# Performance work log

Measured on AMD Instinct MI355X. Metric: run time of the kernel, lower is better.

The kernel has to match this reference:

```python
import jax, jax.numpy as jnp
import numpy as np

PATCH = 16      # sqrt(n_patches=256)
ALPHA = 10.0
HEADS, DH = 2, 64


def _fourier(coords, Bm):
    # coords: (HW, 2), Bm: (n_features, 2) -> (HW, 2*n_features)
    proj = 2.0 * jnp.pi * coords @ Bm.T
    return jnp.concatenate([jnp.cos(proj), jnp.sin(proj)], axis=-1)


def _forward(coords_decoding, tokens, B_q, B_l0, B_l1,
             qW, qb, toqW, tokvW, tooW, toob,
             bwW0, bwb0, bwW1, bwb1,
             modW0, modb0, modW1, modb1,
             hvW0, hvb0, outW0, outb0, outW1, outb1):
    B = coords_decoding.shape[0]
    Hh, Ww = coords_decoding.shape[1], coords_decoding.shape[2]
    coords = coords_decoding.reshape(B, -1, coords_decoding.shape[-1])
    grid = coords[0]                      # (HW, 2); coords_modulation is None -> same grid
    HW = grid.shape[0]
    m = tokens.shape[1]

    # patch indices and spatial bias
    row = jnp.clip((grid[:, 0] * PATCH).astype(jnp.int32), 0, PATCH - 1)
    col = jnp.clip((grid[:, 1] * PATCH).astype(jnp.int32), 0, PATCH - 1)
    idx = row * PATCH + col               # (HW,)
    t = idx.astype(jnp.float32) / (PATCH * PATCH)
    pos = (jnp.arange(m, dtype=jnp.float32) + 0.5) / m
    rel = -ALPHA * jnp.abs(t[None, :] - pos[:, None]) ** 2   # (m, HW)
    bias = rel.T                          # (HW, m), broadcast over batch & heads

    # query features (shared across batch)
    xq = jax.nn.relu(_fourier(grid, B_q) @ qW + qb)           # (HW, hd)
    xq_b = jnp.broadcast_to(xq[None], (B, HW, xq.shape[-1]))

    # cross attention with spatial bias
    q = (xq_b @ toqW).reshape(B, HW, HEADS, DH).transpose(0, 2, 1, 3)   # (B,h,HW,Dh)
    kv = tokens @ tokvW                                                  # (B,m,2*inner)
    k, v = jnp.split(kv, 2, axis=-1)
    k = k.reshape(B, m, HEADS, DH).transpose(0, 2, 1, 3)                 # (B,h,m,Dh)
    v = v.reshape(B, m, HEADS, DH).transpose(0, 2, 1, 3)
    sim = jnp.einsum('bhqd,bhkd->bhqk', q, k) * (DH ** -0.5) + bias[None, None]
    attn = jax.nn.softmax(sim, axis=-1)
    o = jnp.einsum('bhqk,bhkd->bhqd', attn, v)
    o = o.transpose(0, 2, 1, 3).reshape(B, HW, HEADS * DH)
    mod = o @ tooW + toob                                                # (B,HW,hd)

    # per-band MLP stack (layer_num = 2)
    def band(Bl, bwW, bwb, mW, mb):
        h = jax.nn.relu(_fourier(grid, Bl) @ bwW + bwb)                  # (HW,hd)
        return jax.nn.relu(h[None] + mod @ mW + mb)                      # (B,HW,hd)

    m0 = band(B_l0, bwW0, bwb0, modW0, modb0)
    m1 = band(B_l1, bwW1, bwb1, modW1, modb1)
    hv0 = m0
    hv1 = jax.nn.relu((m1 + hv0) @ hvW0 + hvb0)
    out = (hv0 @ outW0 + outb0) + (hv1 @ outW1 + outb1)                  # (B,HW,3)
    return out.reshape(B, Hh, Ww, -1)


def setup_inputs() -> dict:
    key = jax.random.key(0)
    ks = jax.random.split(key, 32)
    B, H, W, L = 4, 128, 128, 256
    fd, hd, cd, od = 64, 256, 256, 3
    nf = fd // 2
    inner = HEADS * DH

    def lin(k, i, o):
        return jax.random.normal(k, (i, o), dtype=jnp.float32) / np.sqrt(i).astype(np.float32)

    inp = {}
    inp['coords_decoding'] = jax.random.uniform(ks[0], (B, H, W, 2), dtype=jnp.float32)
    inp['tokens'] = jax.random.normal(ks[1], (B, L, cd), dtype=jnp.float32)
    inp['B_q'] = jax.random.normal(ks[2], (nf, 2), dtype=jnp.float32) / 16.0
    inp['B_l0'] = jax.random.normal(ks[3], (nf, 2), dtype=jnp.float32) / 128.0
    inp['B_l1'] = jax.random.normal(ks[4], (nf, 2), dtype=jnp.float32) / 32.0
    inp['qW'] = lin(ks[5], fd, hd); inp['qb'] = jnp.zeros((hd,), jnp.float32)
    inp['toqW'] = lin(ks[6], hd, inner)
    inp['tokvW'] = lin(ks[7], cd, inner * 2)
    inp['tooW'] = lin(ks[8], inner, hd); inp['toob'] = jnp.zeros((hd,), jnp.float32)
    inp['bwW0'] = lin(ks[9], fd, hd); inp['bwb0'] = jnp.zeros((hd,), jnp.float32)
    inp['bwW1'] = lin(ks[10], fd, hd); inp['bwb1'] = jnp.zeros((hd,), jnp.float32)
    inp['modW0'] = lin(ks[11], hd, hd); inp['modb0'] = jnp.zeros((hd,), jnp.float32)
    inp['modW1'] = lin(ks[12], hd, hd); inp['modb1'] = jnp.zeros((hd,), jnp.float32)
    inp['hvW0'] = lin(ks[13], hd, hd); inp['hvb0'] = jnp.zeros((hd,), jnp.float32)
    inp['outW0'] = lin(ks[14], hd, od); inp['outb0'] = jnp.zeros((od,), jnp.float32)
    inp['outW1'] = lin(ks[15], hd, od); inp['outb1'] = jnp.zeros((od,), jnp.float32)
    return inp


def reference(coords_decoding, tokens, B_q, B_l0, B_l1,
              qW, qb, toqW, tokvW, tooW, toob,
              bwW0, bwb0, bwW1, bwb1,
              modW0, modb0, modW1, modb1,
              hvW0, hvb0, outW0, outb0, outW1, outb1):
    return _forward(coords_decoding, tokens, B_q, B_l0, B_l1,
                    qW, qb, toqW, tokvW, tooW, toob,
                    bwW0, bwb0, bwW1, bwb1,
                    modW0, modb0, modW1, modb1,
                    hvW0, hvb0, outW0, outb0, outW1, outb1)
```

## Files before the change

kernel.cpp:

```cpp
#include <hip/hip_runtime.h>
#include <stdint.h>

constexpr int kHW = 16384;
constexpr int kB  = 4;
constexpr int kM  = 256;

typedef _Float16 half8 __attribute__((ext_vector_type(8)));
typedef __attribute__((ext_vector_type(4))) float f32x4;

__device__ __forceinline__ unsigned short f2h(float f) {
  _Float16 h = (_Float16)f;
  return __builtin_bit_cast(unsigned short, h);
}
__device__ __forceinline__ float h2f(unsigned short u) {
  return (float)__builtin_bit_cast(_Float16, u);
}

__global__ __launch_bounds__(256) void prep_kernel(
    const float* __restrict__ tokens, const float* __restrict__ tokvW,
    unsigned short* __restrict__ kn_ws, unsigned short* __restrict__ vt_ws,
    const float* __restrict__ tooW, const float* __restrict__ modW0,
    const float* __restrict__ modW1, const float* __restrict__ hvW0,
    const float* __restrict__ qW, const float* __restrict__ bwW0,
    const float* __restrict__ bwW1, const float* __restrict__ toqW,
    unsigned short* __restrict__ tooWt, unsigned short* __restrict__ modW0t,
    unsigned short* __restrict__ modW1t, unsigned short* __restrict__ hvW0t,
    unsigned short* __restrict__ qWt, unsigned short* __restrict__ bw0t,
    unsigned short* __restrict__ bw1t, unsigned short* __restrict__ toqWt)
{
  __shared__ __align__(16) float tok[256];
  int bx = blockIdx.x, tid = threadIdx.x;

  if (bx < kB * kM) {
    int b = bx >> 8, j = bx & 255, c = tid;
    tok[c] = tokens[(b * kM + j) * 256 + c];
    __syncthreads();
    float acc = 0.f;
    for (int i4 = 0; i4 < 64; i4++) {
      float4 t4 = *(const float4*)&tok[i4 * 4];
      acc += t4.x * tokvW[(i4*4+0)*256 + c] + t4.y * tokvW[(i4*4+1)*256 + c]
           + t4.z * tokvW[(i4*4+2)*256 + c] + t4.w * tokvW[(i4*4+3)*256 + c];
    }
    unsigned short hv = f2h(acc);
    if (c < 128) {
      int h = c >> 6, dd = c & 63;
      kn_ws[((size_t)(b*2+h)*256 + j) * 64 + dd] = hv;
    } else {
      int c2 = c - 128;
      int h = c2 >> 6, dd = c2 & 63;
      vt_ws[((size_t)(b*2+h)*64 + dd) * 256 + j] = hv;
    }
  } else {
    int t = bx - kB * kM;
    int m = t >> 3, ch = t & 7;
    const float* Ws[8] = {tooW, modW0, modW1, hvW0, qW, bwW0, bwW1, toqW};
    unsigned short* Wts[8] = {tooWt, modW0t, modW1t, hvW0t, qWt, bw0t, bw1t, toqWt};
    const int Ks[8] = {128, 256, 256, 256, 64, 64, 64, 256};
    const int Ns[8] = {256, 256, 256, 256, 256, 256, 256, 128};
    const float* W = Ws[m];
    unsigned short* Wt = Wts[m];
    int K = Ks[m], N = Ns[m];
    int nkb = K / 8;
    int per = nkb >> 3;
    int kb0 = ch * per;
    if (tid < N) {
      for (int kb = kb0; kb < kb0 + per; kb++) {
        unsigned short sv[8];
#pragma unroll
        for (int i = 0; i < 8; i++)
          sv[i] = f2h(W[(kb * 8 + i) * N + tid]);
        *(uint4*)&Wt[tid * K + kb * 8] = *(const uint4*)sv;
      }
    }
  }
}

constexpr int kFPitch = 72;
constexpr int kXPitch = 264;

__global__ __launch_bounds__(256, 2) void feat_kernel(
    const float* __restrict__ coords,
    const float* __restrict__ Bq, const float* __restrict__ Bl0, const float* __restrict__ Bl1,
    const float* __restrict__ qb, const float* __restrict__ bwb0, const float* __restrict__ bwb1,
    const unsigned short* __restrict__ qWt, const unsigned short* __restrict__ bw0t,
    const unsigned short* __restrict__ bw1t, const unsigned short* __restrict__ toqWt,
    float* __restrict__ t_ws, unsigned short* __restrict__ qc_ws,
    unsigned short* __restrict__ h0_hf, unsigned short* __restrict__ h1_hf)
{
  __shared__ __align__(16) unsigned short ff_s[3][32][kFPitch];
  __shared__ __align__(16) unsigned short xq_s[32][kXPitch];
  __shared__ float coords_s[64];

  int tid = threadIdx.x;
  int px0 = blockIdx.x * 32;
  int w = tid >> 6, ln = tid & 63;
  int c = ln & 15, q = ln >> 4;

  if (tid < 64) coords_s[tid] = coords[px0 * 2 + tid];
  __syncthreads();

#pragma unroll
  for (int r = 0; r < 24; r++) {
    int v = r * 256 + tid;
    int mat = v >> 11;
    int p = (v >> 6) & 31;
    int f = v & 63;
    int fr = f & 31;
    const float* Bm = (mat == 0) ? Bq : (mat == 1 ? Bl0 : Bl1);
    float x = coords_s[p * 2 + 0];
    float y = coords_s[p * 2 + 1];
    float proj = 6.283185307179586f * (x * Bm[fr*2+0] + y * Bm[fr*2+1]);
    float s, cc;
    __sincosf(proj, &s, &cc);
    ff_s[mat][p][f] = f2h((f < 32) ? cc : s);
  }
  if (tid < 32) {
    float x = coords_s[tid * 2 + 0];
    float y = coords_s[tid * 2 + 1];
    int row = min(max((int)(x * 16.0f), 0), 15);
    int col = min(max((int)(y * 16.0f), 0), 15);
    t_ws[px0 + tid] = (float)(row * 16 + col) * (1.0f / 256.0f);
  }
  __syncthreads();

  const f32x4 zero4 = {0.f, 0.f, 0.f, 0.f};

  for (int mat = 0; mat < 3; mat++) {
    const unsigned short* Wt = (mat == 0) ? qWt : (mat == 1 ? bw0t : bw1t);
    const float* bias = (mat == 0) ? qb : (mat == 1 ? bwb0 : bwb1);
    f32x4 acc[8];
#pragma unroll
    for (int i = 0; i < 8; i++) acc[i] = zero4;
#pragma unroll
    for (int ks = 0; ks < 2; ks++) {
      int koff = ks * 32 + q * 8;
      half8 bfr[4];
#pragma unroll
      for (int nt = 0; nt < 4; nt++)
        bfr[nt] = *(const half8*)(Wt + (size_t)(w*64 + nt*16 + c) * 64 + koff);
      half8 afr[2];
#pragma unroll
      for (int mt = 0; mt < 2; mt++)
        afr[mt] = *(const half8*)(&ff_s[mat][mt*16 + c][koff]);
#pragma unroll
      for (int mt = 0; mt < 2; mt++)
#pragma unroll
        for (int nt = 0; nt < 4; nt++)
          acc[mt*4+nt] = __builtin_amdgcn_mfma_f32_16x16x32_f16(afr[mt], bfr[nt], acc[mt*4+nt], 0, 0, 0);
    }
    float bv[4];
#pragma unroll
    for (int nt = 0; nt < 4; nt++) bv[nt] = bias[w*64 + nt*16 + c];
#pragma unroll
    for (int mt = 0; mt < 2; mt++)
#pragma unroll
      for (int nt = 0; nt < 4; nt++)
#pragma unroll
        for (int rg = 0; rg < 4; rg++) {
          int row = mt*16 + q*4 + rg, col = w*64 + nt*16 + c;
          unsigned short hv = f2h(fmaxf(acc[mt*4+nt][rg] + bv[nt], 0.f));
          if (mat == 0)      xq_s[row][col] = hv;
          else if (mat == 1) h0_hf[((size_t)(px0 + row)) * 256 + col] = hv;
          else               h1_hf[((size_t)(px0 + row)) * 256 + col] = hv;
        }
  }
  __syncthreads();

  {
    f32x4 acc2[4];
#pragma unroll
    for (int i = 0; i < 4; i++) acc2[i] = zero4;
#pragma unroll
    for (int kt = 0; kt < 8; kt++) {
      int koff = kt * 32 + q * 8;
      half8 bfr[2];
#pragma unroll
      for (int nt = 0; nt < 2; nt++)
        bfr[nt] = *(const half8*)(toqWt + (size_t)(w*32 + nt*16 + c) * 256 + koff);
      half8 afr[2];
#pragma unroll
      for (int mt = 0; mt < 2; mt++)
        afr[mt] = *(const half8*)(&xq_s[mt*16 + c][koff]);
#pragma unroll
      for (int mt = 0; mt < 2; mt++)
#pragma unroll
        for (int nt = 0; nt < 2; nt++)
          acc2[mt*2+nt] = __builtin_amdgcn_mfma_f32_16x16x32_f16(afr[mt], bfr[nt], acc2[mt*2+nt], 0, 0, 0);
    }
#pragma unroll
    for (int mt = 0; mt < 2; mt++)
#pragma unroll
      for (int nt = 0; nt < 2; nt++)
#pragma unroll
        for (int rg = 0; rg < 4; rg++) {
          int row = mt*16 + q*4 + rg, col = w*32 + nt*16 + c;
          qc_ws[((size_t)(px0 + row)) * 128 + col] = f2h(acc2[mt*2+nt][rg]);
        }
  }
}

constexpr int kPPitch = 264;

__global__ __launch_bounds__(256, 2) void attn_kernel(
    const unsigned short* __restrict__ kn_ws,
    const unsigned short* __restrict__ vt_ws,
    const unsigned short* __restrict__ qc_ws,
    const float* __restrict__ t_ws,
    unsigned short* __restrict__ o_hf)
{
  __shared__ __align__(16) unsigned short P_s[32 * kPPitch];
  __shared__ float t_s[32];
  __shared__ float red_max[32][4];
  __shared__ float red_sum[32][4];

  int b = blockIdx.y;
  int px0 = blockIdx.x * 32;
  int tid = threadIdx.x;
  int w = tid >> 6, ln = tid & 63;
  int c = ln & 15, q = ln >> 4;

  if (tid < 32) t_s[tid] = t_ws[px0 + tid];

  const f32x4 zero4 = {0.f, 0.f, 0.f, 0.f};

  for (int h = 0; h < 2; h++) {
    __syncthreads();

    f32x4 acc[8];
#pragma unroll
    for (int i = 0; i < 8; i++) acc[i] = zero4;
    const unsigned short* kbase = kn_ws + (size_t)(b*2+h) * 256 * 64;
#pragma unroll
    for (int ks = 0; ks < 2; ks++) {
      int koff = ks * 32 + q * 8;
      half8 a0 = *(const half8*)(qc_ws + (size_t)(px0 + c) * 128 + h*64 + koff);
      half8 a1 = *(const half8*)(qc_ws + (size_t)(px0 + 16 + c) * 128 + h*64 + koff);
#pragma unroll
      for (int nt = 0; nt < 4; nt++) {
        half8 bf = *(const half8*)(kbase + (size_t)(w*64 + nt*16 + c) * 64 + koff);
        acc[0*4+nt] = __builtin_amdgcn_mfma_f32_16x16x32_f16(a0, bf, acc[0*4+nt], 0, 0, 0);
        acc[1*4+nt] = __builtin_amdgcn_mfma_f32_16x16x32_f16(a1, bf, acc[1*4+nt], 0, 0, 0);
      }
    }

    float lm[2][4];
#pragma unroll
    for (int mt = 0; mt < 2; mt++)
#pragma unroll
      for (int rg = 0; rg < 4; rg++) {
        int row = mt*16 + q*4 + rg;
        float tv = t_s[row];
        float mx = -1e30f;
#pragma unroll
        for (int nt = 0; nt < 4; nt++) {
          int token = w*64 + nt*16 + c;
          float pos = ((float)token + 0.5f) * (1.0f / 256.0f);
          float db = tv - pos;
          float sb = acc[mt*4+nt][rg] * 0.125f - 10.0f * db * db;
          acc[mt*4+nt][rg] = sb;
          mx = fmaxf(mx, sb);
        }
        lm[mt][rg] = mx;
      }
#pragma unroll
    for (int s = 1; s < 16; s <<= 1)
#pragma unroll
      for (int mt = 0; mt < 2; mt++)
#pragma unroll
        for (int rg = 0; rg < 4; rg++)
          lm[mt][rg] = fmaxf(lm[mt][rg], __shfl_xor(lm[mt][rg], s, 64));
    if (c == 0) {
#pragma unroll
      for (int mt = 0; mt < 2; mt++)
#pragma unroll
        for (int rg = 0; rg < 4; rg++)
          red_max[mt*16 + q*4 + rg][w] = lm[mt][rg];
    }
    __syncthreads();

    float ps[2][4];
#pragma unroll
    for (int mt = 0; mt < 2; mt++)
#pragma unroll
      for (int rg = 0; rg < 4; rg++) {
        int row = mt*16 + q*4 + rg;
        float gm = fmaxf(fmaxf(red_max[row][0], red_max[row][1]),
                         fmaxf(red_max[row][2], red_max[row][3]));
        float sum = 0.f;
#pragma unroll
        for (int nt = 0; nt < 4; nt++) {
          float e = __expf(acc[mt*4+nt][rg] - gm);
          sum += e;
          P_s[row * kPPitch + w*64 + nt*16 + c] = f2h(e);
        }
        ps[mt][rg] = sum;
      }
#pragma unroll
    for (int s = 1; s < 16; s <<= 1)
#pragma unroll
      for (int mt = 0; mt < 2; mt++)
#pragma unroll
        for (int rg = 0; rg < 4; rg++)
          ps[mt][rg] += __shfl_xor(ps[mt][rg], s, 64);
    if (c == 0) {
#pragma unroll
      for (int mt = 0; mt < 2; mt++)
#pragma unroll
        for (int rg = 0; rg < 4; rg++)
          red_sum[mt*16 + q*4 + rg][w] = ps[mt][rg];
    }
    __syncthreads();

    f32x4 oacc[2] = {zero4, zero4};
    const unsigned short* vbase = vt_ws + (size_t)(b*2+h) * 64 * 256;
#pragma unroll
    for (int kt = 0; kt < 8; kt++) {
      int koff = kt * 32 + q * 8;
      half8 bf = *(const half8*)(vbase + (size_t)(w*16 + c) * 256 + koff);
      half8 a0 = *(const half8*)(P_s + (0*16 + c) * kPPitch + koff);
      half8 a1 = *(const half8*)(P_s + (1*16 + c) * kPPitch + koff);
      oacc[0] = __builtin_amdgcn_mfma_f32_16x16x32_f16(a0, bf, oacc[0], 0, 0, 0);
      oacc[1] = __builtin_amdgcn_mfma_f32_16x16x32_f16(a1, bf, oacc[1], 0, 0, 0);
    }
#pragma unroll
    for (int mt = 0; mt < 2; mt++)
#pragma unroll
      for (int rg = 0; rg < 4; rg++) {
        int row = mt*16 + q*4 + rg;
        float rinv = 1.0f / (red_sum[row][0] + red_sum[row][1] +
                             red_sum[row][2] + red_sum[row][3]);
        o_hf[((size_t)(b * kHW + px0 + row)) * 128 + h*64 + w*16 + c] =
            f2h(oacc[mt][rg] * rinv);
      }
  }
}

constexpr int kPitch = 264;

template <int KD>
__device__ __forceinline__ void gemm4(
    const unsigned short* abuf, const unsigned short* wt,
    f32x4* acc , int c, int q)
{
#pragma unroll
  for (int ks = 0; ks < KD / 32; ks++) {
    int koff = ks * 32 + q * 8;
    half8 bfr[4];
#pragma unroll
    for (int nt = 0; nt < 4; nt++)
      bfr[nt] = *(const half8*)(wt + (nt * 16 + c) * KD + koff);
    half8 afr[4];
#pragma unroll
    for (int mt = 0; mt < 4; mt++)
      afr[mt] = *(const half8*)(abuf + (mt * 16 + c) * kPitch + koff);
#pragma unroll
    for (int mt = 0; mt < 4; mt++)
#pragma unroll
      for (int nt = 0; nt < 4; nt++)
        acc[mt * 4 + nt] = __builtin_amdgcn_mfma_f32_16x16x32_f16(afr[mt], bfr[nt], acc[mt * 4 + nt], 0, 0, 0);
  }
}

__global__ __launch_bounds__(256, 2) void mlp_kernel(
    const unsigned short* __restrict__ o_hf,
    const unsigned short* __restrict__ h0_hf, const unsigned short* __restrict__ h1_hf,
    const unsigned short* __restrict__ tooWt, const float* __restrict__ toob,
    const unsigned short* __restrict__ modW0t, const float* __restrict__ modb0,
    const unsigned short* __restrict__ modW1t, const float* __restrict__ modb1,
    const unsigned short* __restrict__ hvW0t, const float* __restrict__ hvb0,
    const float* __restrict__ outW0, const float* __restrict__ outb0,
    const float* __restrict__ outW1, const float* __restrict__ outb1,
    float* __restrict__ dout)
{
  __shared__ __align__(16) unsigned short buf0[64 * kPitch];
  __shared__ __align__(16) unsigned short buf1[64 * kPitch];
  __shared__ __align__(16) unsigned short hbuf[16 * kPitch];
  __shared__ __align__(16) float scratch[64 * 3 * 4];

  int tid = threadIdx.x;
  int px0 = blockIdx.x * 16;
  int w = tid >> 6, ln = tid & 63;
  int c = ln & 15, q = ln >> 4;

#pragma unroll
  for (int i = 0; i < 4; i++) {
    int idx = i * 256 + tid;
    int r = idx >> 4, c8 = (idx & 15) * 8;
    int b = r >> 4, px = r & 15;
    uint4 v = *(const uint4*)(o_hf + ((size_t)(b * kHW + px0 + px)) * 128 + c8);
    *(uint4*)&buf0[r * kPitch + c8] = v;
  }
#pragma unroll
  for (int i = 0; i < 2; i++) {
    int idx = i * 256 + tid;
    int p = idx >> 5, c8 = (idx & 31) * 8;
    uint4 v = *(const uint4*)(h0_hf + ((size_t)(px0 + p)) * 256 + c8);
    *(uint4*)&hbuf[p * kPitch + c8] = v;
  }
  __syncthreads();

  f32x4 acc[16];
  const f32x4 zero4 = {0.f, 0.f, 0.f, 0.f};

#pragma unroll
  for (int i = 0; i < 16; i++) acc[i] = zero4;
  gemm4<128>(buf0, tooWt + (size_t)w * 64 * 128, acc, c, q);
  {
    float bias[4];
#pragma unroll
    for (int nt = 0; nt < 4; nt++) bias[nt] = toob[w * 64 + nt * 16 + c];
#pragma unroll
    for (int mt = 0; mt < 4; mt++)
#pragma unroll
      for (int nt = 0; nt < 4; nt++)
#pragma unroll
        for (int rg = 0; rg < 4; rg++) {
          int row = mt * 16 + q * 4 + rg, col = w * 64 + nt * 16 + c;
          buf1[row * kPitch + col] = f2h(acc[mt * 4 + nt][rg] + bias[nt]);
        }
  }
  __syncthreads();

#pragma unroll
  for (int i = 0; i < 16; i++) acc[i] = zero4;
  gemm4<256>(buf1, modW0t + (size_t)w * 64 * 256, acc, c, q);
  {
    float bias[4], hr[4][4];
#pragma unroll
    for (int nt = 0; nt < 4; nt++) {
      int col = w * 64 + nt * 16 + c;
      bias[nt] = modb0[col];
#pragma unroll
      for (int rg = 0; rg < 4; rg++)
        hr[nt][rg] = h2f(hbuf[(q * 4 + rg) * kPitch + col]);
    }
#pragma unroll
    for (int mt = 0; mt < 4; mt++)
#pragma unroll
      for (int nt = 0; nt < 4; nt++)
#pragma unroll
        for (int rg = 0; rg < 4; rg++) {
          int row = mt * 16 + q * 4 + rg, col = w * 64 + nt * 16 + c;
          buf0[row * kPitch + col] =
              f2h(fmaxf(acc[mt * 4 + nt][rg] + bias[nt] + hr[nt][rg], 0.f));
        }
  }
  __syncthreads();

#pragma unroll
  for (int i = 0; i < 2; i++) {
    int idx = i * 256 + tid;
    int p = idx >> 5, c8 = (idx & 31) * 8;
    uint4 v = *(const uint4*)(h1_hf + ((size_t)(px0 + p)) * 256 + c8);
    *(uint4*)&hbuf[p * kPitch + c8] = v;
  }
#pragma unroll
  for (int i = 0; i < 16; i++) acc[i] = zero4;
  gemm4<256>(buf1, modW1t + (size_t)w * 64 * 256, acc, c, q);
  __syncthreads();
  {
    float bias[4], hr[4][4];
#pragma unroll
    for (int nt = 0; nt < 4; nt++) {
      int col = w * 64 + nt * 16 + c;
      bias[nt] = modb1[col];
#pragma unroll
      for (int rg = 0; rg < 4; rg++)
        hr[nt][rg] = h2f(hbuf[(q * 4 + rg) * kPitch + col]);
    }
#pragma unroll
    for (int mt = 0; mt < 4; mt++)
#pragma unroll
      for (int nt = 0; nt < 4; nt++)
#pragma unroll
        for (int rg = 0; rg < 4; rg++) {
          int row = mt * 16 + q * 4 + rg, col = w * 64 + nt * 16 + c;
          float m0v = h2f(buf0[row * kPitch + col]);
          float v = m0v + fmaxf(acc[mt * 4 + nt][rg] + bias[nt] + hr[nt][rg], 0.f);
          buf1[row * kPitch + col] = f2h(v);
        }
  }
  __syncthreads();

#pragma unroll
  for (int i = 0; i < 16; i++) acc[i] = zero4;
  gemm4<256>(buf1, hvW0t + (size_t)w * 64 * 256, acc, c, q);
  {
    float bias[4], w0v[4][3], w1v[4][3];
#pragma unroll
    for (int nt = 0; nt < 4; nt++) {
      int col = w * 64 + nt * 16 + c;
      bias[nt] = hvb0[col];
#pragma unroll
      for (int k = 0; k < 3; k++) {
        w0v[nt][k] = outW0[col * 3 + k];
        w1v[nt][k] = outW1[col * 3 + k];
      }
    }
#pragma unroll
    for (int mt = 0; mt < 4; mt++) {
      float pk[4][3];
#pragma unroll
      for (int rg = 0; rg < 4; rg++)
#pragma unroll
        for (int k = 0; k < 3; k++) pk[rg][k] = 0.f;
#pragma unroll
      for (int nt = 0; nt < 4; nt++) {
        int col = w * 64 + nt * 16 + c;
#pragma unroll
        for (int rg = 0; rg < 4; rg++) {
          int row = mt * 16 + q * 4 + rg;
          float hv1 = fmaxf(acc[mt * 4 + nt][rg] + bias[nt], 0.f);
          float m0v = h2f(buf0[row * kPitch + col]);
#pragma unroll
          for (int k = 0; k < 3; k++)
            pk[rg][k] += m0v * w0v[nt][k] + hv1 * w1v[nt][k];
        }
      }
#pragma unroll
      for (int s = 1; s < 16; s <<= 1)
#pragma unroll
        for (int rg = 0; rg < 4; rg++)
#pragma unroll
          for (int k = 0; k < 3; k++)
            pk[rg][k] += __shfl_xor(pk[rg][k], s, 64);
      if (c == 0) {
#pragma unroll
        for (int rg = 0; rg < 4; rg++) {
          int row = mt * 16 + q * 4 + rg;
#pragma unroll
          for (int k = 0; k < 3; k++)
            scratch[row * 12 + k * 4 + w] = pk[rg][k];
        }
      }
    }
  }
  __syncthreads();

  if (tid < 192) {
    int row = tid / 3, k = tid % 3;
    int b = row >> 4, px = px0 + (row & 15);
    float s = outb0[k] + outb1[k];
#pragma unroll
    for (int ww = 0; ww < 4; ww++) s += scratch[row * 12 + k * 4 + ww];
    dout[((size_t)b * kHW + px) * 3 + k] = s;
  }
}

extern "C" void kernel_launch(void* const* d_in, const int* in_sizes, int n_in,
                              void* d_out, int out_size, void* d_ws, size_t ws_size,
                              hipStream_t stream) {
  const float* coords = (const float*)d_in[0];
  const float* tokens = (const float*)d_in[1];
  const float* Bq     = (const float*)d_in[2];
  const float* Bl0    = (const float*)d_in[3];
  const float* Bl1    = (const float*)d_in[4];
  const float* qW     = (const float*)d_in[5];
  const float* qb     = (const float*)d_in[6];
  const float* toqW   = (const float*)d_in[7];
  const float* tokvW  = (const float*)d_in[8];
  const float* tooW   = (const float*)d_in[9];
  const float* toob   = (const float*)d_in[10];
  const float* bwW0   = (const float*)d_in[11];
  const float* bwb0   = (const float*)d_in[12];
  const float* bwW1   = (const float*)d_in[13];
  const float* bwb1   = (const float*)d_in[14];
  const float* modW0  = (const float*)d_in[15];
  const float* modb0  = (const float*)d_in[16];
  const float* modW1  = (const float*)d_in[17];
  const float* modb1  = (const float*)d_in[18];
  const float* hvW0   = (const float*)d_in[19];
  const float* hvb0   = (const float*)d_in[20];
  const float* outW0  = (const float*)d_in[21];
  const float* outb0  = (const float*)d_in[22];
  const float* outW1  = (const float*)d_in[23];
  const float* outb1  = (const float*)d_in[24];

  char* ws = (char*)d_ws;
  float*          t_ws   = (float*)(ws + 0);
  unsigned short* qc_ws  = (unsigned short*)(ws + 65536);
  unsigned short* h0_hf  = (unsigned short*)(ws + 4259840);
  unsigned short* h1_hf  = (unsigned short*)(ws + 12648448);
  unsigned short* o_hf   = (unsigned short*)(ws + 21037056);
  unsigned short* kn_ws  = (unsigned short*)(ws + 37814272);
  unsigned short* vt_ws  = (unsigned short*)(ws + 38076416);
  unsigned short* tooWt  = (unsigned short*)(ws + 38338560);
  unsigned short* modW0t = (unsigned short*)(ws + 38404096);
  unsigned short* modW1t = (unsigned short*)(ws + 38535168);
  unsigned short* hvW0t  = (unsigned short*)(ws + 38666240);
  unsigned short* qWt    = (unsigned short*)(ws + 38797312);
  unsigned short* bw0t   = (unsigned short*)(ws + 38830080);
  unsigned short* bw1t   = (unsigned short*)(ws + 38862848);
  unsigned short* toqWt  = (unsigned short*)(ws + 38895616);

  prep_kernel<<<dim3(kB * kM + 64), 256, 0, stream>>>(
      tokens, tokvW, kn_ws, vt_ws,
      tooW, modW0, modW1, hvW0, qW, bwW0, bwW1, toqW,
      tooWt, modW0t, modW1t, hvW0t, qWt, bw0t, bw1t, toqWt);
  feat_kernel<<<dim3(kHW / 32), 256, 0, stream>>>(
      coords, Bq, Bl0, Bl1, qb, bwb0, bwb1,
      qWt, bw0t, bw1t, toqWt,
      t_ws, qc_ws, h0_hf, h1_hf);
  attn_kernel<<<dim3(kHW / 32, kB), 256, 0, stream>>>(kn_ws, vt_ws, qc_ws, t_ws, o_hf);
  mlp_kernel<<<dim3(kHW / 16), 256, 0, stream>>>(
      o_hf, h0_hf, h1_hf, tooWt, toob, modW0t, modb0, modW1t, modb1,
      hvW0t, hvb0, outW0, outb0, outW1, outb1, (float*)d_out);
}
```

Baseline: 243.0 us.

## Fuse feature and attention kernels; keep residual tiles in registers in MLP

Merges feat_kernel and attn_kernel into a single kernel. Each block computes its query features and projected queries into shared memory, then loops over all batches and heads for attention. This removes the qc_ws and t_ws global round trips and one launch, and it reuses a shared-memory arena for the feature and softmax buffers. The MLP kernel now loads h0/h1 straight into registers and keeps the first modulation output as fp16 registers, which drops the hbuf staging and a few barriers. In exchange, the attention grid is four times smaller (only 512 blocks, each doing 4 batches serially), which may cut parallelism, and register pressure in the MLP kernel goes up.

```diff
diff --git a/kernel.cpp b/kernel.cpp
--- a/kernel.cpp
+++ b/kernel.cpp
@@ -75,26 +75,36 @@
   }
 }
 
-constexpr int kFPitch = 72;
-constexpr int kXPitch = 264;
-
-__global__ __launch_bounds__(256, 2) void feat_kernel(
+constexpr int kAPitch = 264;
+constexpr int kQPitch = 136;
+
+__global__ __launch_bounds__(256, 2) void featattn_kernel(
     const float* __restrict__ coords,
     const float* __restrict__ Bq, const float* __restrict__ Bl0, const float* __restrict__ Bl1,
     const float* __restrict__ qb, const float* __restrict__ bwb0, const float* __restrict__ bwb1,
     const unsigned short* __restrict__ qWt, const unsigned short* __restrict__ bw0t,
     const unsigned short* __restrict__ bw1t, const unsigned short* __restrict__ toqWt,
-    float* __restrict__ t_ws, unsigned short* __restrict__ qc_ws,
-    unsigned short* __restrict__ h0_hf, unsigned short* __restrict__ h1_hf)
+    const unsigned short* __restrict__ kn_ws, const unsigned short* __restrict__ vt_ws,
+    unsigned short* __restrict__ h0_hf, unsigned short* __restrict__ h1_hf,
+    unsigned short* __restrict__ o_hf)
 {
-  __shared__ __align__(16) unsigned short ff_s[3][32][kFPitch];
-  __shared__ __align__(16) unsigned short xq_s[32][kXPitch];
+  __shared__ __align__(16) unsigned short arena[15360];
+  __shared__ __align__(16) unsigned short qc_s[32 * kQPitch];
+  __shared__ float t_s[32];
   __shared__ float coords_s[64];
+  __shared__ float red_max[32][4];
+  __shared__ float red_sum[32][4];
+
+  unsigned short* ff  = arena;
+  unsigned short* xq  = arena + 6912;
+  unsigned short* P_s = arena;
 
   int tid = threadIdx.x;
   int px0 = blockIdx.x * 32;
   int w = tid >> 6, ln = tid & 63;
   int c = ln & 15, q = ln >> 4;
+
+  const f32x4 zero4 = {0.f, 0.f, 0.f, 0.f};
 
   if (tid < 64) coords_s[tid] = coords[px0 * 2 + tid];
   __syncthreads();
@@ -112,18 +122,16 @@
     float proj = 6.283185307179586f * (x * Bm[fr*2+0] + y * Bm[fr*2+1]);
     float s, cc;
     __sincosf(proj, &s, &cc);
-    ff_s[mat][p][f] = f2h((f < 32) ? cc : s);
+    ff[(mat * 32 + p) * 72 + f] = f2h((f < 32) ? cc : s);
   }
   if (tid < 32) {
     float x = coords_s[tid * 2 + 0];
     float y = coords_s[tid * 2 + 1];
     int row = min(max((int)(x * 16.0f), 0), 15);
     int col = min(max((int)(y * 16.0f), 0), 15);
-    t_ws[px0 + tid] = (float)(row * 16 + col) * (1.0f / 256.0f);
-  }
-  __syncthreads();
-
-  const f32x4 zero4 = {0.f, 0.f, 0.f, 0.f};
+    t_s[tid] = (float)(row * 16 + col) * (1.0f / 256.0f);
+  }
+  __syncthreads();
 
   for (int mat = 0; mat < 3; mat++) {
     const unsigned short* Wt = (mat == 0) ? qWt : (mat == 1 ? bw0t : bw1t);
@@ -141,7 +149,7 @@
       half8 afr[2];
 #pragma unroll
       for (int mt = 0; mt < 2; mt++)
-        afr[mt] = *(const half8*)(&ff_s[mat][mt*16 + c][koff]);
+        afr[mt] = *(const half8*)(ff + (mat * 32 + mt*16 + c) * 72 + koff);
 #pragma unroll
       for (int mt = 0; mt < 2; mt++)
 #pragma unroll
@@ -159,7 +167,7 @@
         for (int rg = 0; rg < 4; rg++) {
           int row = mt*16 + q*4 + rg, col = w*64 + nt*16 + c;
           unsigned short hv = f2h(fmaxf(acc[mt*4+nt][rg] + bv[nt], 0.f));
-          if (mat == 0)      xq_s[row][col] = hv;
+          if (mat == 0)      xq[row * kAPitch + col] = hv;
           else if (mat == 1) h0_hf[((size_t)(px0 + row)) * 256 + col] = hv;
           else               h1_hf[((size_t)(px0 + row)) * 256 + col] = hv;
         }
@@ -180,7 +188,7 @@
       half8 afr[2];
 #pragma unroll
       for (int mt = 0; mt < 2; mt++)
-        afr[mt] = *(const half8*)(&xq_s[mt*16 + c][koff]);
+        afr[mt] = *(const half8*)(xq + (mt*16 + c) * kAPitch + koff);
 #pragma unroll
       for (int mt = 0; mt < 2; mt++)
 #pragma unroll
@@ -194,144 +202,121 @@
 #pragma unroll
         for (int rg = 0; rg < 4; rg++) {
           int row = mt*16 + q*4 + rg, col = w*32 + nt*16 + c;
-          qc_ws[((size_t)(px0 + row)) * 128 + col] = f2h(acc2[mt*2+nt][rg]);
-        }
-  }
-}
-
-constexpr int kPPitch = 264;
-
-__global__ __launch_bounds__(256, 2) void attn_kernel(
-    const unsigned short* __restrict__ kn_ws,
-    const unsigned short* __restrict__ vt_ws,
-    const unsigned short* __restrict__ qc_ws,
-    const float* __restrict__ t_ws,
-    unsigned short* __restrict__ o_hf)
-{
-  __shared__ __align__(16) unsigned short P_s[32 * kPPitch];
-  __shared__ float t_s[32];
-  __shared__ float red_max[32][4];
-  __shared__ float red_sum[32][4];
-
-  int b = blockIdx.y;
-  int px0 = blockIdx.x * 32;
-  int tid = threadIdx.x;
-  int w = tid >> 6, ln = tid & 63;
-  int c = ln & 15, q = ln >> 4;
-
-  if (tid < 32) t_s[tid] = t_ws[px0 + tid];
-
-  const f32x4 zero4 = {0.f, 0.f, 0.f, 0.f};
-
-  for (int h = 0; h < 2; h++) {
-    __syncthreads();
-
-    f32x4 acc[8];
-#pragma unroll
-    for (int i = 0; i < 8; i++) acc[i] = zero4;
-    const unsigned short* kbase = kn_ws + (size_t)(b*2+h) * 256 * 64;
-#pragma unroll
-    for (int ks = 0; ks < 2; ks++) {
-      int koff = ks * 32 + q * 8;
-      half8 a0 = *(const half8*)(qc_ws + (size_t)(px0 + c) * 128 + h*64 + koff);
-      half8 a1 = *(const half8*)(qc_ws + (size_t)(px0 + 16 + c) * 128 + h*64 + koff);
-#pragma unroll
-      for (int nt = 0; nt < 4; nt++) {
-        half8 bf = *(const half8*)(kbase + (size_t)(w*64 + nt*16 + c) * 64 + koff);
-        acc[0*4+nt] = __builtin_amdgcn_mfma_f32_16x16x32_f16(a0, bf, acc[0*4+nt], 0, 0, 0);
-        acc[1*4+nt] = __builtin_amdgcn_mfma_f32_16x16x32_f16(a1, bf, acc[1*4+nt], 0, 0, 0);
-      }
-    }
-
-    float lm[2][4];
-#pragma unroll
-    for (int mt = 0; mt < 2; mt++)
-#pragma unroll
-      for (int rg = 0; rg < 4; rg++) {
-        int row = mt*16 + q*4 + rg;
-        float tv = t_s[row];
-        float mx = -1e30f;
+          qc_s[row * kQPitch + col] = f2h(acc2[mt*2+nt][rg]);
+        }
+  }
+
+  for (int b = 0; b < kB; b++) {
+    for (int h = 0; h < 2; h++) {
+      __syncthreads();
+
+      f32x4 acc[8];
+#pragma unroll
+      for (int i = 0; i < 8; i++) acc[i] = zero4;
+      const unsigned short* kbase = kn_ws + (size_t)(b*2+h) * 256 * 64;
+#pragma unroll
+      for (int ks = 0; ks < 2; ks++) {
+        int koff = ks * 32 + q * 8;
+        half8 a0 = *(const half8*)(qc_s + c * kQPitch + h*64 + koff);
+        half8 a1 = *(const half8*)(qc_s + (16 + c) * kQPitch + h*64 + koff);
 #pragma unroll
         for (int nt = 0; nt < 4; nt++) {
-          int token = w*64 + nt*16 + c;
-          float pos = ((float)token + 0.5f) * (1.0f / 256.0f);
-          float db = tv - pos;
-          float sb = acc[mt*4+nt][rg] * 0.125f - 10.0f * db * db;
-          acc[mt*4+nt][rg] = sb;
-          mx = fmaxf(mx, sb);
-        }
-        lm[mt][rg] = mx;
-      }
-#pragma unroll
-    for (int s = 1; s < 16; s <<= 1)
-#pragma unroll
-      for (int mt = 0; mt < 2; mt++)
-#pragma unroll
-        for (int rg = 0; rg < 4; rg++)
-          lm[mt][rg] = fmaxf(lm[mt][rg], __shfl_xor(lm[mt][rg], s, 64));
-    if (c == 0) {
-#pragma unroll
-      for (int mt = 0; mt < 2; mt++)
-#pragma unroll
-        for (int rg = 0; rg < 4; rg++)
-          red_max[mt*16 + q*4 + rg][w] = lm[mt][rg];
-    }
-    __syncthreads();
-
-    float ps[2][4];
-#pragma unroll
-    for (int mt = 0; mt < 2; mt++)
-#pragma unroll
-      for (int rg = 0; rg < 4; rg++) {
-        int row = mt*16 + q*4 + rg;
-        float gm = fmaxf(fmaxf(red_max[row][0], red_max[row][1]),
-                         fmaxf(red_max[row][2], red_max[row][3]));
-        float sum = 0.f;
-#pragma unroll
-        for (int nt = 0; nt < 4; nt++) {
-          float e = __expf(acc[mt*4+nt][rg] - gm);
-          sum += e;
-          P_s[row * kPPitch + w*64 + nt*16 + c] = f2h(e);
-        }
-        ps[mt][rg] = sum;
-      }
-#pragma unroll
-    for (int s = 1; s < 16; s <<= 1)
-#pragma unroll
-      for (int mt = 0; mt < 2; mt++)
-#pragma unroll
-        for (int rg = 0; rg < 4; rg++)
-          ps[mt][rg] += __shfl_xor(ps[mt][rg], s, 64);
-    if (c == 0) {
-#pragma unroll
-      for (int mt = 0; mt < 2; mt++)
-#pragma unroll
-        for (int rg = 0; rg < 4; rg++)
-          red_sum[mt*16 + q*4 + rg][w] = ps[mt][rg];
-    }
-    __syncthreads();
-
-    f32x4 oacc[2] = {zero4, zero4};
-    const unsigned short* vbase = vt_ws + (size_t)(b*2+h) * 64 * 256;
-#pragma unroll
-    for (int kt = 0; kt < 8; kt++) {
-      int koff = kt * 32 + q * 8;
-      half8 bf = *(const half8*)(vbase + (size_t)(w*16 + c) * 256 + koff);
-      half8 a0 = *(const half8*)(P_s + (0*16 + c) * kPPitch + koff);
-      half8 a1 = *(const half8*)(P_s + (1*16 + c) * kPPitch + koff);
-      oacc[0] = __builtin_amdgcn_mfma_f32_16x16x32_f16(a0, bf, oacc[0], 0, 0, 0);
-      oacc[1] = __builtin_amdgcn_mfma_f32_16x16x32_f16(a1, bf, oacc[1], 0, 0, 0);
-    }
-#pragma unroll
-    for (int mt = 0; mt < 2; mt++)
-#pragma unroll
-      for (int rg = 0; rg < 4; rg++) {
-        int row = mt*16 + q*4 + rg;
-        float rinv = 1.0f / (red_sum[row][0] + red_sum[row][1] +
-                             red_sum[row][2] + red_sum[row][3]);
-        o_hf[((size_t)(b * kHW + px0 + row)) * 128 + h*64 + w*16 + c] =
-            f2h(oacc[mt][rg] * rinv);
-      }
+          half8 bf = *(const half8*)(kbase + (size_t)(w*64 + nt*16 + c) * 64 + koff);
+          acc[0*4+nt] = __builtin_amdgcn_mfma_f32_16x16x32_f16(a0, bf, acc[0*4+nt], 0, 0, 0);
+          acc[1*4+nt] = __builtin_amdgcn_mfma_f32_16x16x32_f16(a1, bf, acc[1*4+nt], 0, 0, 0);
+        }
+      }
+
+      float lm[2][4];
+#pragma unroll
+      for (int mt = 0; mt < 2; mt++)
+#pragma unroll
+        for (int rg = 0; rg < 4; rg++) {
+          int row = mt*16 + q*4 + rg;
+          float tv = t_s[row];
+          float mx = -1e30f;
+#pragma unroll
+          for (int nt = 0; nt < 4; nt++) {
+            int token = w*64 + nt*16 + c;
+            float pos = ((float)token + 0.5f) * (1.0f / 256.0f);
+            float db = tv - pos;
+            float sb = acc[mt*4+nt][rg] * 0.125f - 10.0f * db * db;
+            acc[mt*4+nt][rg] = sb;
+            mx = fmaxf(mx, sb);
+          }
+          lm[mt][rg] = mx;
+        }
+#pragma unroll
+      for (int s = 1; s < 16; s <<= 1)
+#pragma unroll
+        for (int mt = 0; mt < 2; mt++)
+#pragma unroll
+          for (int rg = 0; rg < 4; rg++)
+            lm[mt][rg] = fmaxf(lm[mt][rg], __shfl_xor(lm[mt][rg], s, 64));
+      if (c == 0) {
+#pragma unroll
+        for (int mt = 0; mt < 2; mt++)
+#pragma unroll
+          for (int rg = 0; rg < 4; rg++)
+            red_max[mt*16 + q*4 + rg][w] = lm[mt][rg];
+      }
+      __syncthreads();
+
+      float ps[2][4];
+#pragma unroll
+      for (int mt = 0; mt < 2; mt++)
+#pragma unroll
+        for (int rg = 0; rg < 4; rg++) {
+          int row = mt*16 + q*4 + rg;
+          float gm = fmaxf(fmaxf(red_max[row][0], red_max[row][1]),
+                           fmaxf(red_max[row][2], red_max[row][3]));
+          float sum = 0.f;
+#pragma unroll
+          for (int nt = 0; nt < 4; nt++) {
+            float e = __expf(acc[mt*4+nt][rg] - gm);
+            sum += e;
+            P_s[row * kAPitch + w*64 + nt*16 + c] = f2h(e);
+          }
+          ps[mt][rg] = sum;
+        }
+#pragma unroll
+      for (int s = 1; s < 16; s <<= 1)
+#pragma unroll
+        for (int mt = 0; mt < 2; mt++)
+#pragma unroll
+          for (int rg = 0; rg < 4; rg++)
+            ps[mt][rg] += __shfl_xor(ps[mt][rg], s, 64);
+      if (c == 0) {
+#pragma unroll
+        for (int mt = 0; mt < 2; mt++)
+#pragma unroll
+          for (int rg = 0; rg < 4; rg++)
+            red_sum[mt*16 + q*4 + rg][w] = ps[mt][rg];
+      }
+      __syncthreads();
+
+      f32x4 oacc[2] = {zero4, zero4};
+      const unsigned short* vbase = vt_ws + (size_t)(b*2+h) * 64 * 256;
+#pragma unroll
+      for (int kt = 0; kt < 8; kt++) {
+        int koff = kt * 32 + q * 8;
+        half8 bf = *(const half8*)(vbase + (size_t)(w*16 + c) * 256 + koff);
+        half8 a0 = *(const half8*)(P_s + (0*16 + c) * kAPitch + koff);
+        half8 a1 = *(const half8*)(P_s + (1*16 + c) * kAPitch + koff);
+        oacc[0] = __builtin_amdgcn_mfma_f32_16x16x32_f16(a0, bf, oacc[0], 0, 0, 0);
+        oacc[1] = __builtin_amdgcn_mfma_f32_16x16x32_f16(a1, bf, oacc[1], 0, 0, 0);
+      }
+#pragma unroll
+      for (int mt = 0; mt < 2; mt++)
+#pragma unroll
+        for (int rg = 0; rg < 4; rg++) {
+          int row = mt*16 + q*4 + rg;
+          float rinv = 1.0f / (red_sum[row][0] + red_sum[row][1] +
+                               red_sum[row][2] + red_sum[row][3]);
+          o_hf[((size_t)(b * kHW + px0 + row)) * 128 + h*64 + w*16 + c] =
+              f2h(oacc[mt][rg] * rinv);
+        }
+    }
   }
 }
 
@@ -374,13 +359,24 @@
 {
   __shared__ __align__(16) unsigned short buf0[64 * kPitch];
   __shared__ __align__(16) unsigned short buf1[64 * kPitch];
-  __shared__ __align__(16) unsigned short hbuf[16 * kPitch];
-  __shared__ __align__(16) float scratch[64 * 3 * 4];
+  __shared__ __align__(16) float scratch[64 * 12];
 
   int tid = threadIdx.x;
   int px0 = blockIdx.x * 16;
   int w = tid >> 6, ln = tid & 63;
   int c = ln & 15, q = ln >> 4;
+
+  unsigned short h0r[4][4], h1r[4][4];
+#pragma unroll
+  for (int nt = 0; nt < 4; nt++) {
+    int col = w * 64 + nt * 16 + c;
+#pragma unroll
+    for (int rg = 0; rg < 4; rg++) {
+      int px = q * 4 + rg;
+      h0r[nt][rg] = h0_hf[((size_t)(px0 + px)) * 256 + col];
+      h1r[nt][rg] = h1_hf[((size_t)(px0 + px)) * 256 + col];
+    }
+  }
 
 #pragma unroll
   for (int i = 0; i < 4; i++) {
@@ -390,13 +386,6 @@
     uint4 v = *(const uint4*)(o_hf + ((size_t)(b * kHW + px0 + px)) * 128 + c8);
     *(uint4*)&buf0[r * kPitch + c8] = v;
   }
-#pragma unroll
-  for (int i = 0; i < 2; i++) {
-    int idx = i * 256 + tid;
-    int p = idx >> 5, c8 = (idx & 31) * 8;
-    uint4 v = *(const uint4*)(h0_hf + ((size_t)(px0 + p)) * 256 + c8);
-    *(uint4*)&hbuf[p * kPitch + c8] = v;
-  }
   __syncthreads();
 
   f32x4 acc[16];
@@ -421,53 +410,31 @@
   }
   __syncthreads();
 
+  _Float16 m0h[4][4][4];
 #pragma unroll
   for (int i = 0; i < 16; i++) acc[i] = zero4;
   gemm4<256>(buf1, modW0t + (size_t)w * 64 * 256, acc, c, q);
   {
-    float bias[4], hr[4][4];
-#pragma unroll
-    for (int nt = 0; nt < 4; nt++) {
-      int col = w * 64 + nt * 16 + c;
-      bias[nt] = modb0[col];
-#pragma unroll
-      for (int rg = 0; rg < 4; rg++)
-        hr[nt][rg] = h2f(hbuf[(q * 4 + rg) * kPitch + col]);
-    }
+    float bias[4];
+#pragma unroll
+    for (int nt = 0; nt < 4; nt++) bias[nt] = modb0[w * 64 + nt * 16 + c];
 #pragma unroll
     for (int mt = 0; mt < 4; mt++)
 #pragma unroll
       for (int nt = 0; nt < 4; nt++)
 #pragma unroll
-        for (int rg = 0; rg < 4; rg++) {
-          int row = mt * 16 + q * 4 + rg, col = w * 64 + nt * 16 + c;
-          buf0[row * kPitch + col] =
-              f2h(fmaxf(acc[mt * 4 + nt][rg] + bias[nt] + hr[nt][rg], 0.f));
-        }
-  }
-  __syncthreads();
-
-#pragma unroll
-  for (int i = 0; i < 2; i++) {
-    int idx = i * 256 + tid;
-    int p = idx >> 5, c8 = (idx & 31) * 8;
-    uint4 v = *(const uint4*)(h1_hf + ((size_t)(px0 + p)) * 256 + c8);
-    *(uint4*)&hbuf[p * kPitch + c8] = v;
-  }
+        for (int rg = 0; rg < 4; rg++)
+          m0h[mt][nt][rg] =
+              (_Float16)fmaxf(acc[mt * 4 + nt][rg] + bias[nt] + h2f(h0r[nt][rg]), 0.f);
+  }
+
 #pragma unroll
   for (int i = 0; i < 16; i++) acc[i] = zero4;
   gemm4<256>(buf1, modW1t + (size_t)w * 64 * 256, acc, c, q);
-  __syncthreads();
   {
-    float bias[4], hr[4][4];
-#pragma unroll
-    for (int nt = 0; nt < 4; nt++) {
-      int col = w * 64 + nt * 16 + c;
-      bias[nt] = modb1[col];
-#pragma unroll
-      for (int rg = 0; rg < 4; rg++)
-        hr[nt][rg] = h2f(hbuf[(q * 4 + rg) * kPitch + col]);
-    }
+    float bias[4];
+#pragma unroll
+    for (int nt = 0; nt < 4; nt++) bias[nt] = modb1[w * 64 + nt * 16 + c];
 #pragma unroll
     for (int mt = 0; mt < 4; mt++)
 #pragma unroll
@@ -475,16 +442,16 @@
 #pragma unroll
         for (int rg = 0; rg < 4; rg++) {
           int row = mt * 16 + q * 4 + rg, col = w * 64 + nt * 16 + c;
-          float m0v = h2f(buf0[row * kPitch + col]);
-          float v = m0v + fmaxf(acc[mt * 4 + nt][rg] + bias[nt] + hr[nt][rg], 0.f);
-          buf1[row * kPitch + col] = f2h(v);
+          float m0v = (float)m0h[mt][nt][rg];
+          float v = m0v + fmaxf(acc[mt * 4 + nt][rg] + bias[nt] + h2f(h1r[nt][rg]), 0.f);
+          buf0[row * kPitch + col] = f2h(v);
         }
   }
   __syncthreads();
 
 #pragma unroll
   for (int i = 0; i < 16; i++) acc[i] = zero4;
-  gemm4<256>(buf1, hvW0t + (size_t)w * 64 * 256, acc, c, q);
+  gemm4<256>(buf0, hvW0t + (size_t)w * 64 * 256, acc, c, q);
   {
     float bias[4], w0v[4][3], w1v[4][3];
 #pragma unroll
@@ -506,12 +473,10 @@
         for (int k = 0; k < 3; k++) pk[rg][k] = 0.f;
 #pragma unroll
       for (int nt = 0; nt < 4; nt++) {
-        int col = w * 64 + nt * 16 + c;
-#pragma unroll
-        for (int rg = 0; rg < 4; rg++) {
-          int row = mt * 16 + q * 4 + rg;
+#pragma unroll
+        for (int rg = 0; rg < 4; rg++) {
           float hv1 = fmaxf(acc[mt * 4 + nt][rg] + bias[nt], 0.f);
-          float m0v = h2f(buf0[row * kPitch + col]);
+          float m0v = (float)m0h[mt][nt][rg];
 #pragma unroll
           for (int k = 0; k < 3; k++)
             pk[rg][k] += m0v * w0v[nt][k] + hv1 * w1v[nt][k];
@@ -577,31 +542,29 @@
   const float* outb1  = (const float*)d_in[24];
 
   char* ws = (char*)d_ws;
-  float*          t_ws   = (float*)(ws + 0);
-  unsigned short* qc_ws  = (unsigned short*)(ws + 65536);
-  unsigned short* h0_hf  = (unsigned short*)(ws + 4259840);
-  unsigned short* h1_hf  = (unsigned short*)(ws + 12648448);
-  unsigned short* o_hf   = (unsigned short*)(ws + 21037056);
-  unsigned short* kn_ws  = (unsigned short*)(ws + 37814272);
-  unsigned short* vt_ws  = (unsigned short*)(ws + 38076416);
-  unsigned short* tooWt  = (unsigned short*)(ws + 38338560);
-  unsigned short* modW0t = (unsigned short*)(ws + 38404096);
-  unsigned short* modW1t = (unsigned short*)(ws + 38535168);
-  unsigned short* hvW0t  = (unsigned short*)(ws + 38666240);
-  unsigned short* qWt    = (unsigned short*)(ws + 38797312);
-  unsigned short* bw0t   = (unsigned short*)(ws + 38830080);
-  unsigned short* bw1t   = (unsigned short*)(ws + 38862848);
-  unsigned short* toqWt  = (unsigned short*)(ws + 38895616);
+  unsigned short* h0_hf  = (unsigned short*)(ws + 0);
+  unsigned short* h1_hf  = (unsigned short*)(ws + 8388608);
+  unsigned short* o_hf   = (unsigned short*)(ws + 16777216);
+  unsigned short* kn_ws  = (unsigned short*)(ws + 33554432);
+  unsigned short* vt_ws  = (unsigned short*)(ws + 33816576);
+  unsigned short* tooWt  = (unsigned short*)(ws + 34078720);
+  unsigned short* modW0t = (unsigned short*)(ws + 34144256);
+  unsigned short* modW1t = (unsigned short*)(ws + 34275328);
+  unsigned short* hvW0t  = (unsigned short*)(ws + 34406400);
+  unsigned short* qWt    = (unsigned short*)(ws + 34537472);
+  unsigned short* bw0t   = (unsigned short*)(ws + 34570240);
+  unsigned short* bw1t   = (unsigned short*)(ws + 34603008);
+  unsigned short* toqWt  = (unsigned short*)(ws + 34635776);
 
   prep_kernel<<<dim3(kB * kM + 64), 256, 0, stream>>>(
       tokens, tokvW, kn_ws, vt_ws,
       tooW, modW0, modW1, hvW0, qW, bwW0, bwW1, toqW,
       tooWt, modW0t, modW1t, hvW0t, qWt, bw0t, bw1t, toqWt);
-  feat_kernel<<<dim3(kHW / 32), 256, 0, stream>>>(
+  featattn_kernel<<<dim3(kHW / 32), 256, 0, stream>>>(
       coords, Bq, Bl0, Bl1, qb, bwb0, bwb1,
       qWt, bw0t, bw1t, toqWt,
-      t_ws, qc_ws, h0_hf, h1_hf);
-  attn_kernel<<<dim3(kHW / 32, kB), 256, 0, stream>>>(kn_ws, vt_ws, qc_ws, t_ws, o_hf);
+      kn_ws, vt_ws,
+      h0_hf, h1_hf, o_hf);
   mlp_kernel<<<dim3(kHW / 16), 256, 0, stream>>>(
       o_hf, h0_hf, h1_hf, tooWt, toob, modW0t, modb0, modW1t, modb1,
       hvW0t, hvb0, outW0, outb0, outW1, outb1, (float*)d_out);
```

Measured after the change: 258.8 us. +6.5%, slower.
